# Kernel optimization log

Measured on AMD Instinct MI355X. Metric: run time of the kernel, lower is better.

The kernel has to match this reference:

```python
import jax, jax.numpy as jnp
import numpy as np

B, V = 8, 128  # batch, cubic volume side


def setup_inputs() -> dict:
    key = jax.random.key(0)
    k1, k2 = jax.random.split(key)
    input_volume1 = jax.random.normal(k1, (B, V, V, V), dtype=jnp.float32)
    input_volume2 = jax.random.normal(k2, (B, V, V, V), dtype=jnp.float32)
    return {"input_volume1": input_volume1, "input_volume2": input_volume2}


def reference(input_volume1, input_volume2):
    # Full circular 3D cross-correlation over all relative shifts:
    #   out[b, t] = sum_r v1[b, r] * v2[b, (r + t) mod V]  (t, r are 3D indices)
    # computed via the convolution theorem with real FFTs.
    axes = (1, 2, 3)
    f1 = jnp.fft.rfftn(input_volume1, axes=axes)          # [B, V, V, V//2+1] complex
    f2 = jnp.fft.rfftn(input_volume2, axes=axes)
    out = jnp.fft.irfftn(f1 * jnp.conj(f2), s=(V, V, V), axes=axes)
    return out.astype(jnp.float32)
```

## Files before the change

kernel.cpp:

```cpp
#include <hip/hip_runtime.h>
#include <math.h>


#define V    128
#define V2   16384
#define V3   2097152
#define NB   8
#define PR1  134
#define PC1  66
#define PR3  134
#define PH3  34
#define SLICE (V * PH3)

__device__ __forceinline__ int bitrev7(int x) {
  return (int)(__brev((unsigned)x) >> 25);
}
__device__ __forceinline__ int negrev(int j) {
  int k = bitrev7(j);
  return bitrev7((V - k) & (V - 1));
}

__device__ __forceinline__ float2 cmul(float2 a, float2 b) {
  return make_float2(a.x * b.x - a.y * b.y, a.x * b.y + a.y * b.x);
}
__device__ __forceinline__ float2 cmulc(float2 a, float2 b) {
  return make_float2(a.x * b.x + a.y * b.y, a.y * b.x - a.x * b.y);
}
__device__ __forceinline__ float2 csqr(float2 a) {
  return make_float2(a.x * a.x - a.y * a.y, 2.0f * a.x * a.y);
}
__device__ __forceinline__ float2 f2add(float2 a, float2 b) {
  return make_float2(a.x + b.x, a.y + b.y);
}
__device__ __forceinline__ float2 f2sub(float2 a, float2 b) {
  return make_float2(a.x - b.x, a.y - b.y);
}
__device__ __forceinline__ float2 NI(float2 z) { return make_float2(z.y, -z.x); }
__device__ __forceinline__ float2 PI(float2 z) { return make_float2(-z.y, z.x); }

#define KC1 0.92387953251128675613f
#define KS1 0.38268343236508977173f
#define KR  0.70710678118654752440f

template <int CTRL>
__device__ __forceinline__ float dppf(float v) {
  return __int_as_float(
      __builtin_amdgcn_update_dpp(0, __float_as_int(v), CTRL, 0xF, 0xF, true));
}
template <int CTRL>
__device__ __forceinline__ float2 dpp2(float2 v) {
  return make_float2(dppf<CTRL>(v.x), dppf<CTRL>(v.y));
}

struct WFT {
  float2 w1, w2, w4, w8, ts4, ts2;
  float sg4, sg2, sg1;
  bool up4, up2;
  int e;

  __device__ void init(int lq) {
    e = lq ^ (((lq >> 2) & 1) * 3);
    const float k = -6.28318530717958647692f / 128.0f;
    w1 = make_float2(cosf(k * (float)e), sinf(k * (float)e));
    w2 = csqr(w1);
    w4 = csqr(w2);
    w8 = csqr(w4);
    up4 = (e >> 2) & 1;
    up2 = (e >> 1) & 1;
    const bool up1 = e & 1;
    sg4 = up4 ? -1.0f : 1.0f;
    sg2 = up2 ? -1.0f : 1.0f;
    sg1 = up1 ? -1.0f : 1.0f;
    const int m4 = e & 3;
    float2 w8p = (m4 == 0) ? make_float2(1.0f, 0.0f)
               : (m4 == 1) ? make_float2(KR, -KR)
               : (m4 == 2) ? make_float2(0.0f, -1.0f)
                           : make_float2(-KR, -KR);
    ts4 = up4 ? w8p : make_float2(1.0f, 0.0f);
    ts2 = (up2 && (e & 1)) ? make_float2(0.0f, -1.0f) : make_float2(1.0f, 0.0f);
  }

  __device__ __forceinline__ void xf4(float2* c, int n) const {
#pragma unroll
    for (int j = 0; j < n; ++j) {
      float2 p = dpp2<0x141>(c[j]);
      float2 t = make_float2(fmaf(c[j].x, sg4, p.x), fmaf(c[j].y, sg4, p.y));
      c[j] = cmul(t, ts4);
    }
#pragma unroll
    for (int j = 0; j < n; ++j) {
      float2 p = dpp2<0x4E>(c[j]);
      float2 t = make_float2(fmaf(c[j].x, sg2, p.x), fmaf(c[j].y, sg2, p.y));
      c[j] = cmul(t, ts2);
    }
#pragma unroll
    for (int j = 0; j < n; ++j) {
      float2 p = dpp2<0xB1>(c[j]);
      c[j] = make_float2(fmaf(c[j].x, sg1, p.x), fmaf(c[j].y, sg1, p.y));
    }
  }
  __device__ __forceinline__ void xi4(float2* c, int n) const {
#pragma unroll
    for (int j = 0; j < n; ++j) {
      float2 p = dpp2<0xB1>(c[j]);
      c[j] = make_float2(fmaf(c[j].x, sg1, p.x), fmaf(c[j].y, sg1, p.y));
    }
#pragma unroll
    for (int j = 0; j < n; ++j) {
      float2 m = cmulc(c[j], ts2);
      float2 q = make_float2(up2 ? m.x : c[j].x, up2 ? m.y : c[j].y);
      float2 p = dpp2<0x4E>(q);
      c[j] = make_float2(fmaf(q.x, sg2, p.x), fmaf(q.y, sg2, p.y));
    }
#pragma unroll
    for (int j = 0; j < n; ++j) {
      float2 m = cmulc(c[j], ts4);
      float2 q = make_float2(up4 ? m.x : c[j].x, up4 ? m.y : c[j].y);
      float2 p = dpp2<0x141>(q);
      c[j] = make_float2(fmaf(q.x, sg4, p.x), fmaf(q.y, sg4, p.y));
    }
  }

  __device__ __forceinline__ void fwd128(float2 c[16]) const {
    const float2 tA = cmul(w1, make_float2(KC1, -KS1));
    const float2 tB = cmul(w1, make_float2(KR, -KR));
    const float2 tC = cmul(w1, make_float2(KS1, -KC1));
#pragma unroll
    for (int j = 0; j < 8; ++j) {
      float2 u = c[j], v = c[j + 8];
      c[j] = f2add(u, v);
      const int q = j & 3;
      float2 tw = (q == 0) ? w1 : (q == 1) ? tA : (q == 2) ? tB : tC;
      float2 t = cmul(f2sub(u, v), tw);
      c[j + 8] = (j < 4) ? t : NI(t);
    }
    const float2 t2 = cmul(w2, make_float2(KR, -KR));
#pragma unroll
    for (int g = 0; g < 2; ++g) {
#pragma unroll
      for (int j0 = 0; j0 < 4; ++j0) {
        const int j = g * 8 + j0;
        float2 u = c[j], v = c[j + 4];
        c[j] = f2add(u, v);
        float2 t = cmul(f2sub(u, v), (j0 & 1) ? t2 : w2);
        c[j + 4] = (j0 < 2) ? t : NI(t);
      }
    }
    const float2 w4n = NI(w4);
#pragma unroll
    for (int g = 0; g < 4; ++g) {
#pragma unroll
      for (int j0 = 0; j0 < 2; ++j0) {
        const int j = g * 4 + j0;
        float2 u = c[j], v = c[j + 2];
        c[j] = f2add(u, v);
        c[j + 2] = cmul(f2sub(u, v), j0 ? w4n : w4);
      }
    }
#pragma unroll
    for (int j = 0; j < 16; j += 2) {
      float2 u = c[j], v = c[j + 1];
      c[j] = f2add(u, v);
      c[j + 1] = cmul(f2sub(u, v), w8);
    }
    xf4(c, 16);
  }

  __device__ __forceinline__ void inv128(float2 c[16]) const {
    xi4(c, 16);
#pragma unroll
    for (int j = 0; j < 16; j += 2) {
      float2 m = cmulc(c[j + 1], w8);
      float2 u = c[j];
      c[j] = f2add(u, m);
      c[j + 1] = f2sub(u, m);
    }
#pragma unroll
    for (int g = 0; g < 4; ++g) {
#pragma unroll
      for (int j0 = 0; j0 < 2; ++j0) {
        const int j = g * 4 + j0;
        float2 m0 = cmulc(c[j + 2], w4);
        float2 m = j0 ? PI(m0) : m0;
        float2 u = c[j];
        c[j] = f2add(u, m);
        c[j + 2] = f2sub(u, m);
      }
    }
    const float2 t2 = cmul(w2, make_float2(KR, -KR));
#pragma unroll
    for (int g = 0; g < 2; ++g) {
#pragma unroll
      for (int j0 = 0; j0 < 4; ++j0) {
        const int j = g * 8 + j0;
        float2 m0 = cmulc(c[j + 4], (j0 & 1) ? t2 : w2);
        float2 m = (j0 < 2) ? m0 : PI(m0);
        float2 u = c[j];
        c[j] = f2add(u, m);
        c[j + 4] = f2sub(u, m);
      }
    }
    const float2 tA = cmul(w1, make_float2(KC1, -KS1));
    const float2 tB = cmul(w1, make_float2(KR, -KR));
    const float2 tC = cmul(w1, make_float2(KS1, -KC1));
#pragma unroll
    for (int j = 0; j < 8; ++j) {
      const int q = j & 3;
      float2 tw = (q == 0) ? w1 : (q == 1) ? tA : (q == 2) ? tB : tC;
      float2 m0 = cmulc(c[j + 8], tw);
      float2 m = (j < 4) ? m0 : PI(m0);
      float2 u = c[j];
      c[j] = f2add(u, m);
      c[j + 8] = f2sub(u, m);
    }
  }

  __device__ __forceinline__ void fwd64(float2 c[8]) const {
    const float2 t2 = cmul(w2, make_float2(KR, -KR));
#pragma unroll
    for (int j = 0; j < 4; ++j) {
      float2 u = c[j], v = c[j + 4];
      c[j] = f2add(u, v);
      float2 t = cmul(f2sub(u, v), (j & 1) ? t2 : w2);
      c[j + 4] = (j < 2) ? t : NI(t);
    }
    const float2 w4n = NI(w4);
#pragma unroll
    for (int g = 0; g < 2; ++g) {
#pragma unroll
      for (int j0 = 0; j0 < 2; ++j0) {
        const int j = g * 4 + j0;
        float2 u = c[j], v = c[j + 2];
        c[j] = f2add(u, v);
        c[j + 2] = cmul(f2sub(u, v), j0 ? w4n : w4);
      }
    }
#pragma unroll
    for (int j = 0; j < 8; j += 2) {
      float2 u = c[j], v = c[j + 1];
      c[j] = f2add(u, v);
      c[j + 1] = cmul(f2sub(u, v), w8);
    }
    xf4(c, 8);
  }
};

__global__ __launch_bounds__(512) void k_fwd_xy(const float* __restrict__ v1,
                                                const float* __restrict__ v2,
                                                float2* __restrict__ Z) {
  __shared__ float2 s[64 * PR1];
  const int tid = threadIdx.x, lane = tid & 63, wave = tid >> 6;
  const int g = tid >> 3, lq = tid & 7;
  const int bz = blockIdx.x >> 1, h = blockIdx.x & 1;
  const int b = bz >> 7, z1 = bz & 127;
  WFT F;
  F.init(lq);
  const int e = F.e;
  const size_t pb = (size_t)b * V3 + (size_t)z1 * V2;
  const float* __restrict__ a1 = v1 + pb + (size_t)g * V;
  const float* __restrict__ a2 = v2 + pb + (size_t)g * V;
  float2 c[16];
  if (h == 0) {
#pragma unroll
    for (int j = 0; j < 16; ++j) {
      const int n = e + 8 * j;
      c[j] = make_float2(a1[n] + a1[n + 64 * V], a2[n] + a2[n + 64 * V]);
    }
  } else {
    const float kk = -6.28318530717958647692f / 128.0f;
    const float2 Wg = make_float2(cosf(kk * (float)g), sinf(kk * (float)g));
#pragma unroll
    for (int j = 0; j < 16; ++j) {
      const int n = e + 8 * j;
      float2 d = make_float2(a1[n] - a1[n + 64 * V], a2[n] - a2[n + 64 * V]);
      c[j] = cmul(d, Wg);
    }
  }
  F.fwd128(c);
#pragma unroll
  for (int j = 0; j < 16; ++j) s[g * PR1 + e + 8 * j] = c[j];
  __syncthreads();
  float2 ca[8], cb[8];
#pragma unroll
  for (int j = 0; j < 8; ++j) {
    const int r = e + 8 * j;
    ca[j] = s[r * PR1 + g];
    cb[j] = s[r * PR1 + g + 64];
  }
  __syncthreads();
  F.fwd64(ca);
  F.fwd64(cb);
#pragma unroll
  for (int j = 0; j < 8; ++j) {
    s[g * PC1 + e + 8 * j] = ca[j];
    s[(g + 64) * PC1 + e + 8 * j] = cb[j];
  }
  __syncthreads();
  for (int L = wave; L < 128; L += 8) {
    const size_t zb = ((size_t)(b * V + L) * V + z1) * V + h * 64;
    Z[zb + lane] = s[L * PC1 + lane];
  }
}

__global__ __launch_bounds__(512) void k_z_fused(float2* __restrict__ Z) {
  __shared__ float2 T[2 * SLICE];
  const int tid = threadIdx.x, lane = tid & 63, wave = tid >> 6;
  const int o = lane >> 3, lq = lane & 7;
  const int blk = blockIdx.x;
  const int b = blk >> 8, idx = blk & 255;
  int x0, x1, jb0, jb1;
  bool within = false;
  {
    const int h = idx >> 7, r2 = idx & 127;
    if (r2 < 126) {
      const int k = (r2 >> 1) + 1, cc = r2 & 1;
      const int xa = bitrev7(k), xb = bitrev7(V - k);
      if (h == 0) { x0 = xa; x1 = xb; jb0 = cc * 32; jb1 = cc * 32; }
      else { x0 = cc ? xb : xa; x1 = cc ? xa : xb; jb0 = 64; jb1 = 96; }
    } else {
      x0 = x1 = r2 - 126;
      if (h == 0) { jb0 = 0; jb1 = 32; within = true; }
      else { jb0 = 64; jb1 = 96; }
    }
  }
  WFT F;
  F.init(lq);
  const int e = F.e;
  const size_t base0 = (size_t)(b * V + x0) * V2 + jb0;
  const size_t base1 = (size_t)(b * V + x1) * V2 + jb1;

  for (int p = tid; p < 2048; p += 512) {
    const int z = p >> 4, w = (p & 15) << 1;
    *(float4*)&T[z * PH3 + w] = *(const float4*)&Z[base0 + (size_t)z * V + w];
  }
  for (int p = tid; p < 2048; p += 512) {
    const int z = p >> 4, w = (p & 15) << 1;
    *(float4*)&T[SLICE + z * PH3 + w] =
        *(const float4*)&Z[base1 + (size_t)z * V + w];
  }
  __syncthreads();

  const int col = wave * 8 + o;
  const int tb = (col >> 5) * SLICE, yc = col & 31;
  float2 c[16];
#pragma unroll
  for (int j = 0; j < 16; ++j) c[j] = T[tb + (e + 8 * j) * PH3 + yc];
  F.fwd128(c);
#pragma unroll
  for (int j = 0; j < 16; ++j) T[tb + (e + 8 * j) * PH3 + yc] = c[j];
  __syncthreads();

  if (!within) {
    for (int p = tid; p < 4096; p += 512) {
      const int z = p >> 5, t = p & 31;
      const int zm = negrev(z), tm = negrev(jb0 + t) & 31;
      const float2 a  = T[z * PH3 + t];
      const float2 bb = T[SLICE + zm * PH3 + tm];
      const float f1r = 0.5f * (a.x + bb.x), f1i = 0.5f * (a.y - bb.y);
      const float f2r = 0.5f * (a.y + bb.y), f2i = 0.5f * (bb.x - a.x);
      const float gr = f1r * f2r + f1i * f2i;
      const float gi = f1i * f2r - f1r * f2i;
      T[z * PH3 + t] = make_float2(gr, gi);
      T[SLICE + zm * PH3 + tm] = make_float2(gr, -gi);
    }
  } else {
    for (int p = tid; p < 8192; p += 512) {
      const int s2 = p >> 12, z = (p >> 5) & 127, t = p & 31;
      const int zm = negrev(z), tm = negrev(s2 * 32 + t) & 31;
      const int pl = z * 32 + t, pm = zm * 32 + tm;
      if (pm < pl) continue;
      const float2 a  = T[s2 * SLICE + z * PH3 + t];
      const float2 bb = T[s2 * SLICE + zm * PH3 + tm];
      const float f1r = 0.5f * (a.x + bb.x), f1i = 0.5f * (a.y - bb.y);
      const float f2r = 0.5f * (a.y + bb.y), f2i = 0.5f * (bb.x - a.x);
      const float gr = f1r * f2r + f1i * f2i;
      const float gi = f1i * f2r - f1r * f2i;
      T[s2 * SLICE + z * PH3 + t] = make_float2(gr, gi);
      if (pm != pl) T[s2 * SLICE + zm * PH3 + tm] = make_float2(gr, -gi);
    }
  }
  __syncthreads();

#pragma unroll
  for (int j = 0; j < 16; ++j) c[j] = T[tb + (e + 8 * j) * PH3 + yc];
  F.inv128(c);
#pragma unroll
  for (int j = 0; j < 16; ++j) T[tb + (e + 8 * j) * PH3 + yc] = c[j];
  __syncthreads();

  for (int p = tid; p < 2048; p += 512) {
    const int z = p >> 4, w = (p & 15) << 1;
    *(float4*)&Z[base0 + (size_t)z * V + w] = *(const float4*)&T[z * PH3 + w];
  }
  for (int p = tid; p < 2048; p += 512) {
    const int z = p >> 4, w = (p & 15) << 1;
    *(float4*)&Z[base1 + (size_t)z * V + w] =
        *(const float4*)&T[SLICE + z * PH3 + w];
  }
}

__global__ __launch_bounds__(1024) void k_inv_xy(const float2* __restrict__ Z,
                                                 float* __restrict__ out) {
  __shared__ float2 s[V * PR3];
  const int tid = threadIdx.x, lane = tid & 63, wave = tid >> 6;
  const int g = tid >> 3, lq = tid & 7;
  const int b = blockIdx.x >> 7, z1 = blockIdx.x & 127;
  WFT F;
  F.init(lq);
  const int e = F.e;
  float2 c[16];
  {
    const size_t zb = ((size_t)(b * V + g) * V + z1) * V;
#pragma unroll
    for (int j = 0; j < 16; ++j) c[j] = Z[zb + e + 8 * j];
    F.inv128(c);
#pragma unroll
    for (int j = 0; j < 16; ++j) s[(e + 8 * j) * PR3 + g] = c[j];
  }
  __syncthreads();
  const float sc = 1.0f / 2097152.0f;
  {
#pragma unroll
    for (int j = 0; j < 16; ++j) c[j] = s[g * PR3 + e + 8 * j];
    F.inv128(c);
    float* fr = (float*)(s + g * PR3);
#pragma unroll
    for (int j = 0; j < 16; ++j)
      fr[e + 8 * j] = c[j].x * sc;
  }
  __syncthreads();
  for (int r = wave; r < 128; r += 16) {
    const size_t gg = (size_t)b * V3 + (size_t)z1 * V2 + (size_t)r * V;
    *(float2*)&out[gg + 2 * lane] =
        *(const float2*)((const float*)(s + r * PR3) + 2 * lane);
  }
}

extern "C" void kernel_launch(void* const* d_in, const int* in_sizes, int n_in,
                              void* d_out, int out_size, void* d_ws, size_t ws_size,
                              hipStream_t stream) {
  const float* v1 = (const float*)d_in[0];
  const float* v2 = (const float*)d_in[1];
  float* out = (float*)d_out;
  float2* Z  = (float2*)d_ws;

  k_fwd_xy<<<NB * V * 2, 512, 0, stream>>>(v1, v2, Z);
  k_z_fused<<<NB * 256, 512, 0, stream>>>(Z);
  k_inv_xy<<<NB * V, 1024, 0, stream>>>(Z, out);
}
```

Before: 303.1 us.

## Split xy FFT kernels into quadrant/half blocks with smaller shared memory

The forward xy kernel now splits each z-slice into four quadrant blocks. Each block does the first radix-2 stage of the 128-point x-FFT itself, then runs two 64-point FFTs instead of a 128-point one. The inverse xy kernel splits each slice into two 512-thread blocks, each producing half of the output rows. This cuts shared memory per block and doubles or quadruples the block count, to raise occupancy and parallelism. The cost is that input loads and the first-stage inverse FFTs are repeated across blocks.

```diff
diff --git a/kernel.cpp b/kernel.cpp
--- a/kernel.cpp
+++ b/kernel.cpp
@@ -6,9 +6,8 @@
 #define V2   16384
 #define V3   2097152
 #define NB   8
-#define PR1  134
-#define PC1  66
-#define PR3  134
+#define PQ   66
+#define P3Q  130
 #define PH3  34
 #define SLICE (V * PH3)
 
@@ -121,51 +120,6 @@
     }
   }
 
-  __device__ __forceinline__ void fwd128(float2 c[16]) const {
-    const float2 tA = cmul(w1, make_float2(KC1, -KS1));
-    const float2 tB = cmul(w1, make_float2(KR, -KR));
-    const float2 tC = cmul(w1, make_float2(KS1, -KC1));
-#pragma unroll
-    for (int j = 0; j < 8; ++j) {
-      float2 u = c[j], v = c[j + 8];
-      c[j] = f2add(u, v);
-      const int q = j & 3;
-      float2 tw = (q == 0) ? w1 : (q == 1) ? tA : (q == 2) ? tB : tC;
-      float2 t = cmul(f2sub(u, v), tw);
-      c[j + 8] = (j < 4) ? t : NI(t);
-    }
-    const float2 t2 = cmul(w2, make_float2(KR, -KR));
-#pragma unroll
-    for (int g = 0; g < 2; ++g) {
-#pragma unroll
-      for (int j0 = 0; j0 < 4; ++j0) {
-        const int j = g * 8 + j0;
-        float2 u = c[j], v = c[j + 4];
-        c[j] = f2add(u, v);
-        float2 t = cmul(f2sub(u, v), (j0 & 1) ? t2 : w2);
-        c[j + 4] = (j0 < 2) ? t : NI(t);
-      }
-    }
-    const float2 w4n = NI(w4);
-#pragma unroll
-    for (int g = 0; g < 4; ++g) {
-#pragma unroll
-      for (int j0 = 0; j0 < 2; ++j0) {
-        const int j = g * 4 + j0;
-        float2 u = c[j], v = c[j + 2];
-        c[j] = f2add(u, v);
-        c[j + 2] = cmul(f2sub(u, v), j0 ? w4n : w4);
-      }
-    }
-#pragma unroll
-    for (int j = 0; j < 16; j += 2) {
-      float2 u = c[j], v = c[j + 1];
-      c[j] = f2add(u, v);
-      c[j + 1] = cmul(f2sub(u, v), w8);
-    }
-    xf4(c, 16);
-  }
-
   __device__ __forceinline__ void inv128(float2 c[16]) const {
     xi4(c, 16);
 #pragma unroll
@@ -215,18 +169,34 @@
     }
   }
 
-  __device__ __forceinline__ void fwd64(float2 c[8]) const {
+  __device__ __forceinline__ void fwd128(float2 c[16]) const {
+    const float2 tA = cmul(w1, make_float2(KC1, -KS1));
+    const float2 tB = cmul(w1, make_float2(KR, -KR));
+    const float2 tC = cmul(w1, make_float2(KS1, -KC1));
+#pragma unroll
+    for (int j = 0; j < 8; ++j) {
+      float2 u = c[j], v = c[j + 8];
+      c[j] = f2add(u, v);
+      const int q = j & 3;
+      float2 tw = (q == 0) ? w1 : (q == 1) ? tA : (q == 2) ? tB : tC;
+      float2 t = cmul(f2sub(u, v), tw);
+      c[j + 8] = (j < 4) ? t : NI(t);
+    }
     const float2 t2 = cmul(w2, make_float2(KR, -KR));
 #pragma unroll
-    for (int j = 0; j < 4; ++j) {
-      float2 u = c[j], v = c[j + 4];
-      c[j] = f2add(u, v);
-      float2 t = cmul(f2sub(u, v), (j & 1) ? t2 : w2);
-      c[j + 4] = (j < 2) ? t : NI(t);
+    for (int g = 0; g < 2; ++g) {
+#pragma unroll
+      for (int j0 = 0; j0 < 4; ++j0) {
+        const int j = g * 8 + j0;
+        float2 u = c[j], v = c[j + 4];
+        c[j] = f2add(u, v);
+        float2 t = cmul(f2sub(u, v), (j0 & 1) ? t2 : w2);
+        c[j + 4] = (j0 < 2) ? t : NI(t);
+      }
     }
     const float2 w4n = NI(w4);
 #pragma unroll
-    for (int g = 0; g < 2; ++g) {
+    for (int g = 0; g < 4; ++g) {
 #pragma unroll
       for (int j0 = 0; j0 < 2; ++j0) {
         const int j = g * 4 + j0;
@@ -236,6 +206,35 @@
       }
     }
 #pragma unroll
+    for (int j = 0; j < 16; j += 2) {
+      float2 u = c[j], v = c[j + 1];
+      c[j] = f2add(u, v);
+      c[j + 1] = cmul(f2sub(u, v), w8);
+    }
+    xf4(c, 16);
+  }
+
+  __device__ __forceinline__ void fwd64(float2 c[8]) const {
+    const float2 t2 = cmul(w2, make_float2(KR, -KR));
+#pragma unroll
+    for (int j = 0; j < 4; ++j) {
+      float2 u = c[j], v = c[j + 4];
+      c[j] = f2add(u, v);
+      float2 t = cmul(f2sub(u, v), (j & 1) ? t2 : w2);
+      c[j + 4] = (j < 2) ? t : NI(t);
+    }
+    const float2 w4n = NI(w4);
+#pragma unroll
+    for (int g = 0; g < 2; ++g) {
+#pragma unroll
+      for (int j0 = 0; j0 < 2; ++j0) {
+        const int j = g * 4 + j0;
+        float2 u = c[j], v = c[j + 2];
+        c[j] = f2add(u, v);
+        c[j + 2] = cmul(f2sub(u, v), j0 ? w4n : w4);
+      }
+    }
+#pragma unroll
     for (int j = 0; j < 8; j += 2) {
       float2 u = c[j], v = c[j + 1];
       c[j] = f2add(u, v);
@@ -248,11 +247,13 @@
 __global__ __launch_bounds__(512) void k_fwd_xy(const float* __restrict__ v1,
                                                 const float* __restrict__ v2,
                                                 float2* __restrict__ Z) {
-  __shared__ float2 s[64 * PR1];
+  __shared__ float2 s[64 * PQ];
   const int tid = threadIdx.x, lane = tid & 63, wave = tid >> 6;
   const int g = tid >> 3, lq = tid & 7;
-  const int bz = blockIdx.x >> 1, h = blockIdx.x & 1;
-  const int b = bz >> 7, z1 = bz & 127;
+  const int r8 = blockIdx.x & 7, quad = (blockIdx.x >> 3) & 3;
+  const int unit = (blockIdx.x >> 5) * 8 + r8;
+  const int hx = quad & 1, hy = quad >> 1;
+  const int b = unit >> 7, z1 = unit & 127;
   WFT F;
   F.init(lq);
   const int e = F.e;
@@ -260,7 +261,7 @@
   const float* __restrict__ a1 = v1 + pb + (size_t)g * V;
   const float* __restrict__ a2 = v2 + pb + (size_t)g * V;
   float2 c[16];
-  if (h == 0) {
+  if (hy == 0) {
 #pragma unroll
     for (int j = 0; j < 16; ++j) {
       const int n = e + 8 * j;
@@ -276,29 +277,39 @@
       c[j] = cmul(d, Wg);
     }
   }
-  F.fwd128(c);
-#pragma unroll
-  for (int j = 0; j < 16; ++j) s[g * PR1 + e + 8 * j] = c[j];
-  __syncthreads();
-  float2 ca[8], cb[8];
-#pragma unroll
-  for (int j = 0; j < 8; ++j) {
-    const int r = e + 8 * j;
-    ca[j] = s[r * PR1 + g];
-    cb[j] = s[r * PR1 + g + 64];
-  }
-  __syncthreads();
-  F.fwd64(ca);
-  F.fwd64(cb);
-#pragma unroll
-  for (int j = 0; j < 8; ++j) {
-    s[g * PC1 + e + 8 * j] = ca[j];
-    s[(g + 64) * PC1 + e + 8 * j] = cb[j];
-  }
-  __syncthreads();
-  for (int L = wave; L < 128; L += 8) {
-    const size_t zb = ((size_t)(b * V + L) * V + z1) * V + h * 64;
-    Z[zb + lane] = s[L * PC1 + lane];
+  float2 d[8];
+  if (hx == 0) {
+#pragma unroll
+    for (int j = 0; j < 8; ++j) d[j] = f2add(c[j], c[j + 8]);
+  } else {
+    const float2 tA = cmul(F.w1, make_float2(KC1, -KS1));
+    const float2 tB = cmul(F.w1, make_float2(KR, -KR));
+    const float2 tC = cmul(F.w1, make_float2(KS1, -KC1));
+#pragma unroll
+    for (int j = 0; j < 8; ++j) {
+      float2 u = f2sub(c[j], c[j + 8]);
+      const int q = j & 3;
+      float2 tw = (q == 0) ? F.w1 : (q == 1) ? tA : (q == 2) ? tB : tC;
+      float2 t = cmul(u, tw);
+      d[j] = (j < 4) ? t : NI(t);
+    }
+  }
+  F.fwd64(d);
+#pragma unroll
+  for (int j = 0; j < 8; ++j) s[g * PQ + e + 8 * j] = d[j];
+  __syncthreads();
+  float2 cc[8];
+#pragma unroll
+  for (int j = 0; j < 8; ++j) cc[j] = s[(e + 8 * j) * PQ + g];
+  __syncthreads();
+  F.fwd64(cc);
+#pragma unroll
+  for (int j = 0; j < 8; ++j) s[g * PQ + e + 8 * j] = cc[j];
+  __syncthreads();
+  for (int L = wave; L < 64; L += 8) {
+    const size_t zb =
+        ((size_t)(b * V + hx * 64 + L) * V + z1) * V + hy * 64;
+    Z[zb + lane] = s[L * PQ + lane];
   }
 }
 
@@ -399,40 +410,45 @@
   }
 }
 
-__global__ __launch_bounds__(1024) void k_inv_xy(const float2* __restrict__ Z,
-                                                 float* __restrict__ out) {
-  __shared__ float2 s[V * PR3];
+__global__ __launch_bounds__(512) void k_inv_xy(const float2* __restrict__ Z,
+                                                float* __restrict__ out) {
+  __shared__ float2 s[64 * P3Q];
   const int tid = threadIdx.x, lane = tid & 63, wave = tid >> 6;
   const int g = tid >> 3, lq = tid & 7;
-  const int b = blockIdx.x >> 7, z1 = blockIdx.x & 127;
+  const int r8 = blockIdx.x & 7, hp = (blockIdx.x >> 3) & 1;
+  const int unit = (blockIdx.x >> 4) * 8 + r8;
+  const int b = unit >> 7, z1 = unit & 127;
   WFT F;
   F.init(lq);
   const int e = F.e;
   float2 c[16];
-  {
-    const size_t zb = ((size_t)(b * V + g) * V + z1) * V;
+#pragma unroll 1
+  for (int half = 0; half < 2; ++half) {
+    const int x = g + 64 * half;
+    const size_t zb = ((size_t)(b * V + x) * V + z1) * V;
 #pragma unroll
     for (int j = 0; j < 16; ++j) c[j] = Z[zb + e + 8 * j];
     F.inv128(c);
 #pragma unroll
-    for (int j = 0; j < 16; ++j) s[(e + 8 * j) * PR3 + g] = c[j];
+    for (int jj = 0; jj < 8; ++jj)
+      s[(e + 8 * jj) * P3Q + x] = c[jj + 8 * hp];
   }
   __syncthreads();
   const float sc = 1.0f / 2097152.0f;
   {
 #pragma unroll
-    for (int j = 0; j < 16; ++j) c[j] = s[g * PR3 + e + 8 * j];
+    for (int j = 0; j < 16; ++j) c[j] = s[g * P3Q + e + 8 * j];
     F.inv128(c);
-    float* fr = (float*)(s + g * PR3);
-#pragma unroll
-    for (int j = 0; j < 16; ++j)
-      fr[e + 8 * j] = c[j].x * sc;
-  }
-  __syncthreads();
-  for (int r = wave; r < 128; r += 16) {
-    const size_t gg = (size_t)b * V3 + (size_t)z1 * V2 + (size_t)r * V;
+    float* fr = (float*)(s + g * P3Q);
+#pragma unroll
+    for (int j = 0; j < 16; ++j) fr[e + 8 * j] = c[j].x * sc;
+  }
+  __syncthreads();
+  for (int r = wave; r < 64; r += 8) {
+    const size_t gg =
+        (size_t)b * V3 + (size_t)z1 * V2 + (size_t)(hp * 64 + r) * V;
     *(float2*)&out[gg + 2 * lane] =
-        *(const float2*)((const float*)(s + r * PR3) + 2 * lane);
+        *(const float2*)((const float*)(s + r * P3Q) + 2 * lane);
   }
 }
 
@@ -444,7 +460,7 @@
   float* out = (float*)d_out;
   float2* Z  = (float2*)d_ws;
 
-  k_fwd_xy<<<NB * V * 2, 512, 0, stream>>>(v1, v2, Z);
+  k_fwd_xy<<<NB * V * 4, 512, 0, stream>>>(v1, v2, Z);
   k_z_fused<<<NB * 256, 512, 0, stream>>>(Z);
-  k_inv_xy<<<NB * V, 1024, 0, stream>>>(Z, out);
-}
+  k_inv_xy<<<NB * V * 2, 512, 0, stream>>>(Z, out);
+}
```

Result: slower. 406.1 us (+34.0%).

## Split inverse XY kernel into half-slice blocks with smaller shared memory

Applied to the files above, without the earlier changes.

The inverse XY kernel now launches twice as many 512-thread blocks, each handling half of a z-slice's output rows. Each block recomputes all 128 first-stage inverse FFT rows but stores only the half of frequencies it needs, which roughly halves shared memory per block. The aim is higher occupancy and better latency hiding. The cost is doubled global reads of Z and doubled first-pass FFT work.

```diff
diff --git a/kernel.cpp b/kernel.cpp
--- a/kernel.cpp
+++ b/kernel.cpp
@@ -8,7 +8,7 @@
 #define NB   8
 #define PR1  134
 #define PC1  66
-#define PR3  134
+#define P3Q  130
 #define PH3  34
 #define SLICE (V * PH3)
 
@@ -399,40 +399,49 @@
   }
 }
 
-__global__ __launch_bounds__(1024) void k_inv_xy(const float2* __restrict__ Z,
-                                                 float* __restrict__ out) {
-  __shared__ float2 s[V * PR3];
+__global__ __launch_bounds__(512) void k_inv_xy(const float2* __restrict__ Z,
+                                                float* __restrict__ out) {
+  __shared__ float2 s[64 * P3Q];
   const int tid = threadIdx.x, lane = tid & 63, wave = tid >> 6;
   const int g = tid >> 3, lq = tid & 7;
-  const int b = blockIdx.x >> 7, z1 = blockIdx.x & 127;
+  const int r8 = blockIdx.x & 7, hp = (blockIdx.x >> 3) & 1;
+  const int unit = (blockIdx.x >> 4) * 8 + r8;
+  const int b = unit >> 7, z1 = unit & 127;
   WFT F;
   F.init(lq);
   const int e = F.e;
   float2 c[16];
-  {
-    const size_t zb = ((size_t)(b * V + g) * V + z1) * V;
+#pragma unroll 1
+  for (int half = 0; half < 2; ++half) {
+    const int x = g + 64 * half;
+    const size_t zb = ((size_t)(b * V + x) * V + z1) * V;
 #pragma unroll
     for (int j = 0; j < 16; ++j) c[j] = Z[zb + e + 8 * j];
     F.inv128(c);
-#pragma unroll
-    for (int j = 0; j < 16; ++j) s[(e + 8 * j) * PR3 + g] = c[j];
+    if (hp == 0) {
+#pragma unroll
+      for (int jj = 0; jj < 8; ++jj) s[(e + 8 * jj) * P3Q + x] = c[jj];
+    } else {
+#pragma unroll
+      for (int jj = 0; jj < 8; ++jj) s[(e + 8 * jj) * P3Q + x] = c[jj + 8];
+    }
   }
   __syncthreads();
   const float sc = 1.0f / 2097152.0f;
   {
 #pragma unroll
-    for (int j = 0; j < 16; ++j) c[j] = s[g * PR3 + e + 8 * j];
+    for (int j = 0; j < 16; ++j) c[j] = s[g * P3Q + e + 8 * j];
     F.inv128(c);
-    float* fr = (float*)(s + g * PR3);
-#pragma unroll
-    for (int j = 0; j < 16; ++j)
-      fr[e + 8 * j] = c[j].x * sc;
-  }
-  __syncthreads();
-  for (int r = wave; r < 128; r += 16) {
-    const size_t gg = (size_t)b * V3 + (size_t)z1 * V2 + (size_t)r * V;
+    float* fr = (float*)(s + g * P3Q);
+#pragma unroll
+    for (int j = 0; j < 16; ++j) fr[e + 8 * j] = c[j].x * sc;
+  }
+  __syncthreads();
+  for (int r = wave; r < 64; r += 8) {
+    const size_t gg =
+        (size_t)b * V3 + (size_t)z1 * V2 + (size_t)(hp * 64 + r) * V;
     *(float2*)&out[gg + 2 * lane] =
-        *(const float2*)((const float*)(s + r * PR3) + 2 * lane);
+        *(const float2*)((const float*)(s + r * P3Q) + 2 * lane);
   }
 }
 
@@ -446,5 +455,5 @@
 
   k_fwd_xy<<<NB * V * 2, 512, 0, stream>>>(v1, v2, Z);
   k_z_fused<<<NB * 256, 512, 0, stream>>>(Z);
-  k_inv_xy<<<NB * V, 1024, 0, stream>>>(Z, out);
-}
+  k_inv_xy<<<NB * V * 2, 512, 0, stream>>>(Z, out);
+}
```

Measured after the change: 304.1 us. Within noise of the previous version (+0.3%).
